# Kernel tuning notes

Hardware: AMD Instinct MI355X
Metric: run time of the kernel (lower is better)

## Reference

```python
import jax, jax.numpy as jnp
import numpy as np

FREQUENCY_COUNT = 16

def setup_inputs() -> dict:
    key = jax.random.key(0)
    k1, k2 = jax.random.split(key)
    x = jax.random.normal(k1, (4096, 1024), dtype=jnp.float32)
    coef = jax.random.normal(k2, (1024, 1024, 2 * FREQUENCY_COUNT + 1), dtype=jnp.float32) * 0.1
    return {"x": x, "coef": coef}

def _fourier_features(x, K):
    ks = jnp.arange(1, K + 1, dtype=x.dtype)            # [K]
    ang = x[:, :, None] * ks[None, None, :]             # [B, I, K]
    ones = jnp.ones(x.shape + (1,), dtype=x.dtype)      # [B, I, 1]
    return jnp.concatenate([jnp.sin(ang), jnp.cos(ang), ones], axis=2)

def reference(x, coef):
    K = (coef.shape[-1] - 1) // 2
    values = _fourier_features(x, K)                     # [B, I, 2K+1]
    # sum over input dim i and frequency dim k, weighted per output j
    return jnp.einsum("oik,bik->bo", coef, values)      # [B, O]
```

## Files before the change

kernel.cpp:

```cpp
#include <hip/hip_runtime.h>


#define O_COLS 1024
#define I_DIM  1024
#define NF33   33
#define B_ROWS 4096

#define CW2_BYTES  ((size_t)32 * 2048 * 512 * 2)
#define XT_OFF     (CW2_BYTES)
#define XT_BYTES   ((size_t)I_DIM * B_ROWS * 4)
#define BK_OFF     (XT_OFF + XT_BYTES)
#define BK_BYTES   ((size_t)I_DIM * O_COLS * 4)
#define BIAS_OFF   (BK_OFF + BK_BYTES)
#define PART_OFF   (BIAS_OFF + (1 << 20))
#define PART_BYTES ((size_t)B_ROWS * O_COLS * 4)
#define NEED_T1    (PART_OFF + 3 * PART_BYTES)
#define NEED_T2    (BIAS_OFF + 4096)

#define ASTR 36

typedef _Float16 half8 __attribute__((ext_vector_type(8)));
typedef float f32x16 __attribute__((ext_vector_type(16)));
typedef float float4v __attribute__((ext_vector_type(4)));
union H8 { half8 v; _Float16 h[8]; };

#define BAR() asm volatile("s_waitcnt lgkmcnt(0)\n\ts_barrier" ::: "memory")

__device__ __forceinline__ int ksrc_of(int f) {
  return (f >= 32) ? 32 : ((f >> 1) + ((f & 1) ? 16 : 0));
}

__global__ __launch_bounds__(256)
void convert_coef2(const float* __restrict__ coef, _Float16* __restrict__ Cw2,
                   float* __restrict__ bk) {
  const int gtid = blockIdx.x * 256 + threadIdx.x;
  const int o = gtid & 1023;
  const int i = gtid >> 10;

  const float* src = coef + (size_t)o * (I_DIM * NF33) + (size_t)i * NF33;
  float r[NF33];
#pragma unroll
  for (int k = 0; k < NF33; ++k) r[k] = src[k];

  const int ob32 = o >> 5;
#pragma unroll
  for (int kcl = 0; kcl < 2; ++kcl) {
#pragma unroll
    for (int kh = 0; kh < 2; ++kh) {
      H8 h;
#pragma unroll
      for (int e = 0; e < 8; ++e)
        h.h[e] = (_Float16)r[ksrc_of(kcl * 16 + kh * 8 + e)];
      const size_t blob = (size_t)ob32 * 2048 + (size_t)i * 2 + kcl;
      *(half8*)(Cw2 + blob * 512 + (kh * 32 + (o & 31)) * 8) = h.v;
    }
  }
  bk[(size_t)i * 1024 + o] = r[32];
}

__global__ __launch_bounds__(256)
void transpose_x(const float* __restrict__ x, float* __restrict__ xT) {
  __shared__ float t[64][65];
  const int bi = blockIdx.x;
  const int bj = blockIdx.y;
  const int tx = threadIdx.x & 63, ty = threadIdx.x >> 6;
#pragma unroll
  for (int mq = 0; mq < 16; ++mq) {
    const int r = mq * 4 + ty;
    t[r][tx] = x[(size_t)(bj * 64 + r) * I_DIM + bi * 64 + tx];
  }
  __syncthreads();
#pragma unroll
  for (int mq = 0; mq < 16; ++mq) {
    const int r = mq * 4 + ty;
    xT[(size_t)(bi * 64 + r) * B_ROWS + bj * 64 + tx] = t[tx][r];
  }
}

__global__ __launch_bounds__(256)
void bias_from_bk(const float* __restrict__ bk, float* __restrict__ bias) {
  const int o = blockIdx.x * 256 + threadIdx.x;
  float s0 = 0.f, s1 = 0.f, s2 = 0.f, s3 = 0.f;
  for (int i = 0; i < 1024; i += 4) {
    s0 += bk[(size_t)i * 1024 + o];
    s1 += bk[(size_t)(i + 1) * 1024 + o];
    s2 += bk[(size_t)(i + 2) * 1024 + o];
    s3 += bk[(size_t)(i + 3) * 1024 + o];
  }
  bias[o] = (s0 + s1) + (s2 + s3);
}

__global__ __launch_bounds__(256)
void reduce_parts(float* __restrict__ out, const float* __restrict__ p0,
                  const float* __restrict__ p1, const float* __restrict__ p2) {
  const size_t i = ((size_t)blockIdx.x * 256 + threadIdx.x) * 4;
  float4v a = *(float4v*)(out + i);
  float4v b = *(const float4v*)(p0 + i);
  float4v c = *(const float4v*)(p1 + i);
  float4v d = *(const float4v*)(p2 + i);
  *(float4v*)(out + i) = a + b + c + d;
}

template <bool ATOMIC>
__global__ __launch_bounds__(256, 2)
void fourier_gemm6(const float* __restrict__ xT, const _Float16* __restrict__ Cw2,
                   const float* __restrict__ bias, float* __restrict__ out,
                   float* __restrict__ part) {
  __shared__ _Float16 As[2][2][128][ASTR];

  const int tid = threadIdx.x, lane = tid & 63, wc = tid >> 6;

  const int bid = blockIdx.x;
  const int g = bid & 15;
  const int m0 = (bid >> 4) * 128;
  const int n = g >> 2;
  const int kb = g & 3;
  const int o0 = n * 256;
  const int i0 = kb * 256;

  const int r32 = lane & 31, kh = lane >> 5;

  const int grow = tid & 127;
  const int gcl = tid >> 7;
  const float* pxg = xT + (size_t)(i0 + gcl) * B_ROWS + (m0 + grow);

  const _Float16* pb0 = Cw2 + ((size_t)(n * 8 + wc * 2 + 0) * 2048 + (size_t)i0 * 2) * 512 + lane * 8;
  const _Float16* pb1 = Cw2 + ((size_t)(n * 8 + wc * 2 + 1) * 2048 + (size_t)i0 * 2) * 512 + lane * 8;

  f32x16 acc[4][2];
#pragma unroll
  for (int fr = 0; fr < 4; ++fr)
#pragma unroll
    for (int fc = 0; fc < 2; ++fc)
#pragma unroll
      for (int q = 0; q < 16; ++q) acc[fr][fc][q] = 0.f;
  if (kb == 0) {
#pragma unroll
    for (int fc = 0; fc < 2; ++fc) {
      const float bv = bias[o0 + wc * 64 + fc * 32 + r32];
#pragma unroll
      for (int fr = 0; fr < 4; ++fr)
#pragma unroll
        for (int q = 0; q < 16; ++q) acc[fr][fc][q] = bv;
    }
  }

  auto genA = [&](int bn, float xv) {
    float s1, c1;
    __sincosf(xv, &s1, &c1);
    float s = s1, c = c1;
    _Float16* dst = &As[bn][gcl][grow][0];
#pragma unroll
    for (int c4 = 0; c4 < 4; ++c4) {
      H8 h;
#pragma unroll
      for (int q = 0; q < 4; ++q) {
        h.h[2 * q] = (_Float16)s; h.h[2 * q + 1] = (_Float16)c;
        const float ns = s * c1 + c * s1;
        c = c * c1 - s * s1;
        s = ns;
      }
      *(half8*)(dst + c4 * 8) = h.v;
    }
  };

  auto loadB = [&](half8 (&Bt)[4], int s) {
    const size_t base = (size_t)(s * 2) * 512;
    Bt[0] = *(const half8*)(pb0 + base);
    Bt[1] = *(const half8*)(pb0 + base + 512);
    Bt[2] = *(const half8*)(pb1 + base);
    Bt[3] = *(const half8*)(pb1 + base + 512);
  };

  auto compute = [&](int bn, int col, const half8 (&Bt)[4]) {
    half8 a_[4][2];
#pragma unroll
    for (int fr = 0; fr < 4; ++fr)
#pragma unroll
      for (int kcl = 0; kcl < 2; ++kcl)
        a_[fr][kcl] = *(const half8*)&As[bn][col][fr * 32 + r32][(kcl * 2 + kh) * 8];
    __builtin_amdgcn_s_setprio(1);
#pragma unroll
    for (int kcl = 0; kcl < 2; ++kcl)
#pragma unroll
      for (int fr = 0; fr < 4; ++fr)
#pragma unroll
        for (int fc = 0; fc < 2; ++fc)
          acc[fr][fc] = __builtin_amdgcn_mfma_f32_32x32x16_f16(
              a_[fr][kcl], Bt[fc * 2 + kcl], acc[fr][fc], 0, 0, 0);
    __builtin_amdgcn_s_setprio(0);
  };

  half8 B0[4], B1[4];

  genA(0, pxg[0]);
  float xg = pxg[(size_t)2 * B_ROWS];
  loadB(B0, 0);
  BAR();

#pragma unroll 1
  for (int p = 0; p < 128; ++p) {
    const int buf = p & 1;
    const int s = 2 * p;
    const float xn = pxg[(size_t)(s + 4) * B_ROWS];

    loadB(B1, s + 1);
    compute(buf, 0, B0);
    genA(buf ^ 1, xg);
    loadB(B0, s + 2);
    compute(buf, 1, B1);
    BAR();
    xg = xn;
  }

  float* dst;
  if (ATOMIC) dst = out;
  else dst = (kb == 0) ? out : part + (size_t)(kb - 1) * (B_ROWS * O_COLS);
#pragma unroll
  for (int fr = 0; fr < 4; ++fr)
#pragma unroll
    for (int fc = 0; fc < 2; ++fc)
#pragma unroll
      for (int q = 0; q < 16; ++q) {
        const int row = m0 + fr * 32 + (q & 3) + 8 * (q >> 2) + 4 * kh;
        const int col = o0 + wc * 64 + fc * 32 + r32;
        if (ATOMIC) atomicAdd(&dst[(size_t)row * O_COLS + col], acc[fr][fc][q]);
        else dst[(size_t)row * O_COLS + col] = acc[fr][fc][q];
      }
}

__global__ __launch_bounds__(512, 4)
void fourier_gemm_direct(const float* __restrict__ x, const float* __restrict__ coef,
                         float* __restrict__ out) {
  __shared__ _Float16 Asd[128 * 64];
  __shared__ _Float16 Bsd[128 * 64];

  const int tid = threadIdx.x;
  const int lane = tid & 63;
  const int wave = tid >> 6;
  const int wr = wave >> 1;
  const int wcd = wave & 1;

  const int bid = blockIdx.x;
  const int o0 = (bid & 7) * 128;
  const int kb = (bid >> 3) & 1;
  const int m0 = (bid >> 4) * 128;

  const int rowA = tid >> 3;
  const int cch = tid & 7;
  const int cswz = cch ^ (rowA & 7);
  const int n1 = tid >> 3;
  const int c1q = tid & 7;
  const int r16 = lane & 15;
  const int kq = lane >> 4;

  float4v acc[2][4];
#pragma unroll
  for (int fr = 0; fr < 2; ++fr)
#pragma unroll
    for (int fc = 0; fc < 4; ++fc) acc[fr][fc] = (float4v){0.f, 0.f, 0.f, 0.f};

  float s1a[8], c1a[8], sa[8], ca[8];
  float s1b[8], c1b[8], sb[8], cb[8];

  const float* xa_base = x + (size_t)(m0 + rowA) * I_DIM + (size_t)kb * 512 + cch * 8;
  const float* xb_base = xa_base + (size_t)64 * I_DIM;

#pragma unroll 1
  for (int ib2 = 0; ib2 < 8; ++ib2) {
    {
      const float* xa = xa_base + ib2 * 64;
      const float* xb = xb_base + ib2 * 64;
      float xva[8], xvb[8];
      *(float4*)&xva[0] = *(const float4*)(xa);
      *(float4*)&xva[4] = *(const float4*)(xa + 4);
      *(float4*)&xvb[0] = *(const float4*)(xb);
      *(float4*)&xvb[4] = *(const float4*)(xb + 4);
#pragma unroll
      for (int e = 0; e < 8; ++e) {
        __sincosf(xva[e], &s1a[e], &c1a[e]); sa[e] = s1a[e]; ca[e] = c1a[e];
        __sincosf(xvb[e], &s1b[e], &c1b[e]); sb[e] = s1b[e]; cb[e] = c1b[e];
      }
    }
#pragma unroll 1
    for (int f = 0; f < NF33; ++f) {
      H8 ha, hb;
      if (f == 32) {
#pragma unroll
        for (int e = 0; e < 8; ++e) { ha.h[e] = (_Float16)1.0f; hb.h[e] = (_Float16)1.0f; }
      } else if ((f & 1) == 0) {
#pragma unroll
        for (int e = 0; e < 8; ++e) { ha.h[e] = (_Float16)sa[e]; hb.h[e] = (_Float16)sb[e]; }
      } else {
#pragma unroll
        for (int e = 0; e < 8; ++e) { ha.h[e] = (_Float16)ca[e]; hb.h[e] = (_Float16)cb[e]; }
      }
      __syncthreads();
      {
        const int ks = ksrc_of(f);
        const int ibg = kb * 8 + ib2;
        H8 b1, b2;
#pragma unroll
        for (int e = 0; e < 8; ++e) {
          const size_t ii = (size_t)(ibg * 64 + c1q * 8 + e) * NF33 + ks;
          b1.h[e] = (_Float16)coef[(size_t)(o0 + n1) * (I_DIM * NF33) + ii];
          b2.h[e] = (_Float16)coef[(size_t)(o0 + n1 + 64) * (I_DIM * NF33) + ii];
        }
        const int cs = (c1q ^ (n1 & 7)) << 3;
        *(half8*)&Bsd[n1 * 64 + cs] = b1.v;
        *(half8*)&Bsd[(n1 + 64) * 64 + cs] = b2.v;
      }
      *(half8*)&Asd[rowA * 64 + cswz * 8] = ha.v;
      *(half8*)&Asd[(rowA + 64) * 64 + cswz * 8] = hb.v;
      if ((f & 1) && (f + 2 < NF33)) {
#pragma unroll
        for (int e = 0; e < 8; ++e) {
          float ns = sa[e] * c1a[e] + ca[e] * s1a[e];
          ca[e] = ca[e] * c1a[e] - sa[e] * s1a[e]; sa[e] = ns;
          float nsb = sb[e] * c1b[e] + cb[e] * s1b[e];
          cb[e] = cb[e] * c1b[e] - sb[e] * s1b[e]; sb[e] = nsb;
        }
      }
      __syncthreads();
#pragma unroll
      for (int ksu = 0; ksu < 2; ++ksu) {
        const int ch = ((ksu << 2) + kq) ^ (r16 & 7);
        half8 af[2], bf[4];
#pragma unroll
        for (int fr = 0; fr < 2; ++fr)
          af[fr] = *(const half8*)&Asd[(wr * 32 + fr * 16 + r16) * 64 + ch * 8];
#pragma unroll
        for (int fc = 0; fc < 4; ++fc)
          bf[fc] = *(const half8*)&Bsd[(wcd * 64 + fc * 16 + r16) * 64 + ch * 8];
#pragma unroll
        for (int fr = 0; fr < 2; ++fr)
#pragma unroll
          for (int fc = 0; fc < 4; ++fc)
            acc[fr][fc] = __builtin_amdgcn_mfma_f32_16x16x32_f16(
                af[fr], bf[fc], acc[fr][fc], 0, 0, 0);
      }
    }
  }
#pragma unroll
  for (int fr = 0; fr < 2; ++fr)
#pragma unroll
    for (int fc = 0; fc < 4; ++fc)
#pragma unroll
      for (int r = 0; r < 4; ++r) {
        const int row = m0 + wr * 32 + fr * 16 + kq * 4 + r;
        const int col = o0 + wcd * 64 + fc * 16 + r16;
        atomicAdd(&out[(size_t)row * O_COLS + col], acc[fr][fc][r]);
      }
}

extern "C" void kernel_launch(void* const* d_in, const int* in_sizes, int n_in,
                              void* d_out, int out_size, void* d_ws, size_t ws_size,
                              hipStream_t stream) {
  const float* x = (const float*)d_in[0];
  const float* coef = (const float*)d_in[1];
  float* out = (float*)d_out;

  if (ws_size >= NEED_T1 || ws_size >= NEED_T2) {
    _Float16* Cw2 = (_Float16*)d_ws;
    float* xT   = (float*)((char*)d_ws + XT_OFF);
    float* bk   = (float*)((char*)d_ws + BK_OFF);
    float* bias = (float*)((char*)d_ws + BIAS_OFF);
    convert_coef2<<<dim3(4096), dim3(256), 0, stream>>>(coef, Cw2, bk);
    transpose_x<<<dim3(16, 64), dim3(256), 0, stream>>>(x, xT);
    bias_from_bk<<<dim3(4), dim3(256), 0, stream>>>(bk, bias);
    if (ws_size >= NEED_T1) {
      float* part = (float*)((char*)d_ws + PART_OFF);
      fourier_gemm6<false><<<dim3(512), dim3(256), 0, stream>>>(xT, Cw2, bias, out, part);
      reduce_parts<<<dim3(4096), dim3(256), 0, stream>>>(
          out, part, part + (size_t)B_ROWS * O_COLS, part + (size_t)2 * B_ROWS * O_COLS);
    } else {
      hipMemsetAsync(out, 0, (size_t)B_ROWS * O_COLS * sizeof(float), stream);
      fourier_gemm6<true><<<dim3(512), dim3(256), 0, stream>>>(xT, Cw2, bias, out, nullptr);
    }
  } else {
    hipMemsetAsync(out, 0, (size_t)B_ROWS * O_COLS * sizeof(float), stream);
    fourier_gemm_direct<<<dim3(512), dim3(512), 0, stream>>>(x, coef, out);
  }
}
```

Baseline: 453.9 us.

## Deepen A-tile double buffer to four columns and use shorter-chain harmonic generation

The shared A buffer now holds four input columns per stage instead of two, so the loop runs 64 iterations with one barrier each instead of 128. That halves barrier count, and the sine/cosine feature generation for the next stage is moved to just before the last MFMA group of the iteration. The harmonic recurrence is replaced by double-angle and addition formulas that build all 16 harmonics with a shallower dependency chain. The s_setprio hints around the MFMA block are removed. The cost is doubled LDS use per block and more live registers for the S/C arrays, which may pressure occupancy at the two-blocks-per-SIMD launch bound.

```diff
diff --git a/kernel.cpp b/kernel.cpp
--- a/kernel.cpp
+++ b/kernel.cpp
@@ -103,10 +103,10 @@
 
 template <bool ATOMIC>
 __global__ __launch_bounds__(256, 2)
-void fourier_gemm6(const float* __restrict__ xT, const _Float16* __restrict__ Cw2,
+void fourier_gemm7(const float* __restrict__ xT, const _Float16* __restrict__ Cw2,
                    const float* __restrict__ bias, float* __restrict__ out,
                    float* __restrict__ part) {
-  __shared__ _Float16 As[2][2][128][ASTR];
+  __shared__ _Float16 As[2][4][128][ASTR];
 
   const int tid = threadIdx.x, lane = tid & 63, wc = tid >> 6;
 
@@ -121,8 +121,9 @@
   const int r32 = lane & 31, kh = lane >> 5;
 
   const int grow = tid & 127;
-  const int gcl = tid >> 7;
-  const float* pxg = xT + (size_t)(i0 + gcl) * B_ROWS + (m0 + grow);
+  const int gcw = tid >> 7;
+  const float* pxa = xT + (size_t)(i0 + gcw) * B_ROWS + (m0 + grow);
+  const float* pxb = pxa + (size_t)2 * B_ROWS;
 
   const _Float16* pb0 = Cw2 + ((size_t)(n * 8 + wc * 2 + 0) * 2048 + (size_t)i0 * 2) * 512 + lane * 8;
   const _Float16* pb1 = Cw2 + ((size_t)(n * 8 + wc * 2 + 1) * 2048 + (size_t)i0 * 2) * 512 + lane * 8;
@@ -145,25 +146,35 @@
     }
   }
 
-  auto genA = [&](int bn, float xv) {
-    float s1, c1;
-    __sincosf(xv, &s1, &c1);
-    float s = s1, c = c1;
-    _Float16* dst = &As[bn][gcl][grow][0];
+  auto genH = [&](float xv, _Float16* dst) {
+    float S[17], C[17];
+    __sincosf(xv, &S[1], &C[1]);
+    S[2] = 2.f * S[1] * C[1];  C[2] = fmaf(-2.f * S[1], S[1], 1.f);
+    S[3] = S[2] * C[1] + C[2] * S[1];  C[3] = C[2] * C[1] - S[2] * S[1];
+    S[4] = 2.f * S[2] * C[2];  C[4] = fmaf(-2.f * S[2], S[2], 1.f);
+    S[5] = S[4] * C[1] + C[4] * S[1];  C[5] = C[4] * C[1] - S[4] * S[1];
+    S[6] = S[4] * C[2] + C[4] * S[2];  C[6] = C[4] * C[2] - S[4] * S[2];
+    S[7] = S[4] * C[3] + C[4] * S[3];  C[7] = C[4] * C[3] - S[4] * S[3];
+    S[8] = 2.f * S[4] * C[4];  C[8] = fmaf(-2.f * S[4], S[4], 1.f);
+#pragma unroll
+    for (int k = 1; k < 8; ++k) {
+      S[8 + k] = S[8] * C[k] + C[8] * S[k];
+      C[8 + k] = C[8] * C[k] - S[8] * S[k];
+    }
+    S[16] = 2.f * S[8] * C[8];  C[16] = fmaf(-2.f * S[8], S[8], 1.f);
 #pragma unroll
     for (int c4 = 0; c4 < 4; ++c4) {
       H8 h;
 #pragma unroll
       for (int q = 0; q < 4; ++q) {
-        h.h[2 * q] = (_Float16)s; h.h[2 * q + 1] = (_Float16)c;
-        const float ns = s * c1 + c * s1;
-        c = c * c1 - s * s1;
-        s = ns;
+        const int k = c4 * 4 + q + 1;
+        h.h[2 * q] = (_Float16)S[k];  h.h[2 * q + 1] = (_Float16)C[k];
       }
       *(half8*)(dst + c4 * 8) = h.v;
     }
   };
 
+  half8 B0[4], B1[4];
   auto loadB = [&](half8 (&Bt)[4], int s) {
     const size_t base = (size_t)(s * 2) * 512;
     Bt[0] = *(const half8*)(pb0 + base);
@@ -179,7 +190,6 @@
 #pragma unroll
       for (int kcl = 0; kcl < 2; ++kcl)
         a_[fr][kcl] = *(const half8*)&As[bn][col][fr * 32 + r32][(kcl * 2 + kh) * 8];
-    __builtin_amdgcn_s_setprio(1);
 #pragma unroll
     for (int kcl = 0; kcl < 2; ++kcl)
 #pragma unroll
@@ -188,29 +198,36 @@
         for (int fc = 0; fc < 2; ++fc)
           acc[fr][fc] = __builtin_amdgcn_mfma_f32_32x32x16_f16(
               a_[fr][kcl], Bt[fc * 2 + kcl], acc[fr][fc], 0, 0, 0);
-    __builtin_amdgcn_s_setprio(0);
   };
 
-  half8 B0[4], B1[4];
-
-  genA(0, pxg[0]);
-  float xg = pxg[(size_t)2 * B_ROWS];
+  {
+    const float xa0 = pxa[0], xb0 = pxb[0];
+    genH(xa0, &As[0][gcw][grow][0]);
+    genH(xb0, &As[0][gcw + 2][grow][0]);
+  }
+  float xa = pxa[(size_t)4 * B_ROWS], xb = pxb[(size_t)4 * B_ROWS];
   loadB(B0, 0);
   BAR();
 
 #pragma unroll 1
-  for (int p = 0; p < 128; ++p) {
+  for (int p = 0; p < 64; ++p) {
     const int buf = p & 1;
-    const int s = 2 * p;
-    const float xn = pxg[(size_t)(s + 4) * B_ROWS];
+    const int s = 4 * p;
+    const float xan = pxa[(size_t)(s + 8) * B_ROWS];
+    const float xbn = pxb[(size_t)(s + 8) * B_ROWS];
 
     loadB(B1, s + 1);
     compute(buf, 0, B0);
-    genA(buf ^ 1, xg);
     loadB(B0, s + 2);
     compute(buf, 1, B1);
+    loadB(B1, s + 3);
+    compute(buf, 2, B0);
+    if (p < 63) loadB(B0, s + 4);
+    genH(xa, &As[buf ^ 1][gcw][grow][0]);
+    genH(xb, &As[buf ^ 1][gcw + 2][grow][0]);
+    compute(buf, 3, B1);
     BAR();
-    xg = xn;
+    xa = xan; xb = xbn;
   }
 
   float* dst;
@@ -370,12 +387,12 @@
     bias_from_bk<<<dim3(4), dim3(256), 0, stream>>>(bk, bias);
     if (ws_size >= NEED_T1) {
       float* part = (float*)((char*)d_ws + PART_OFF);
-      fourier_gemm6<false><<<dim3(512), dim3(256), 0, stream>>>(xT, Cw2, bias, out, part);
+      fourier_gemm7<false><<<dim3(512), dim3(256), 0, stream>>>(xT, Cw2, bias, out, part);
       reduce_parts<<<dim3(4096), dim3(256), 0, stream>>>(
           out, part, part + (size_t)B_ROWS * O_COLS, part + (size_t)2 * B_ROWS * O_COLS);
     } else {
       hipMemsetAsync(out, 0, (size_t)B_ROWS * O_COLS * sizeof(float), stream);
-      fourier_gemm6<true><<<dim3(512), dim3(256), 0, stream>>>(xT, Cw2, bias, out, nullptr);
+      fourier_gemm7<true><<<dim3(512), dim3(256), 0, stream>>>(xT, Cw2, bias, out, nullptr);
     }
   } else {
     hipMemsetAsync(out, 0, (size_t)B_ROWS * O_COLS * sizeof(float), stream);
```

Result: no change. 450.2 us (-0.8%).
